# Performance work log

Hardware: AMD Instinct MI355X
Metric: run time of the kernel (lower is better)

Reference implementation:

```python
import jax, jax.numpy as jnp
import numpy as np

SCALING = 32.0 / 16.0  # alpha / r

def setup_inputs() -> dict:
    key = jax.random.key(0)
    k1, k2, k3, k4 = jax.random.split(key, 4)
    B_, S, D_in, D_out, R = 4, 2048, 4096, 4096, 16
    x = jax.random.normal(k1, (B_, S, D_in), dtype=jnp.float32)
    W_base = jax.random.normal(k2, (D_out, D_in), dtype=jnp.float32) * 0.02
    b_base = jax.random.normal(k3, (D_out,), dtype=jnp.float32) * 0.02
    A = jax.random.normal(k4, (R, D_in), dtype=jnp.float32) * 0.02
    B = jnp.zeros((D_out, R), dtype=jnp.float32)  # lora_B init to zeros
    return {"x": x, "W_base": W_base, "b_base": b_base, "A": A, "B": B}

def reference(x, W_base, b_base, A, B):
    # base linear (stands in for dequantized 4-bit matmul): [B,S,Din] @ [Din,Dout]
    out = jnp.einsum('bsd,od->bso', x, W_base) + b_base
    # LoRA path: B(A(x)) * scaling, dropout=0 -> identity
    xa = jnp.einsum('bsd,rd->bsr', x, A)        # [B,S,r]
    delta = jnp.einsum('bsr,or->bso', xa, B)    # [B,S,Dout]
    return out + delta * SCALING
```

## Files before the change

### kernel.cpp

```cpp
#include <hip/hip_runtime.h>


typedef __attribute__((ext_vector_type(4))) float f32x4;
typedef __attribute__((ext_vector_type(8))) short bf16x8;

__device__ __forceinline__ unsigned short f2bf(float f) {
    unsigned u = __builtin_bit_cast(unsigned, f);
    unsigned r = u + 0x7fffu + ((u >> 16) & 1u);
    return (unsigned short)(r >> 16);
}

__device__ __forceinline__ void gload_lds16(const void* g, void* l) {
    __builtin_amdgcn_global_load_lds(
        (const __attribute__((address_space(1))) void*)g,
        (__attribute__((address_space(3))) void*)l, 16, 0, 0);
}

__global__ __launch_bounds__(256) void cast_x_kernel(
    const float* __restrict__ x, unsigned short* __restrict__ xb, int n8)
{
    int stride = gridDim.x * blockDim.x;
    for (int i = blockIdx.x * blockDim.x + threadIdx.x; i < n8; i += stride) {
        size_t base = (size_t)i * 8;
        float4 f0 = *(const float4*)&x[base];
        float4 f1 = *(const float4*)&x[base + 4];
        ushort4 o0, o1;
        o0.x = f2bf(f0.x); o0.y = f2bf(f0.y); o0.z = f2bf(f0.z); o0.w = f2bf(f0.w);
        o1.x = f2bf(f1.x); o1.y = f2bf(f1.y); o1.z = f2bf(f1.z); o1.w = f2bf(f1.w);
        *(ushort4*)&xb[base]     = o0;
        *(ushort4*)&xb[base + 4] = o1;
    }
}

__global__ __launch_bounds__(256) void prep_w_kernel(
    const float* __restrict__ W, const float* __restrict__ A,
    const float* __restrict__ Bl, unsigned short* __restrict__ wb,
    int K, float scale)
{
    __shared__ float Bs[16][16];
    const int t = threadIdx.x;
    const int n0 = blockIdx.y * 16;
    const int k0 = blockIdx.x * 256;
    {
        int nl = t >> 4, r = t & 15;
        Bs[nl][r] = Bl[(size_t)(n0 + nl) * 16 + r];
    }
    __syncthreads();

    const int lane = t & 63;
    const int wv = t >> 6;
    const int k = k0 + lane * 4;

    float4 av[16];
#pragma unroll
    for (int r = 0; r < 16; ++r)
        av[r] = *(const float4*)&A[(size_t)r * K + k];

#pragma unroll
    for (int j = 0; j < 4; ++j) {
        const int nl = wv * 4 + j;
        const int n = n0 + nl;
        float4 w = *(const float4*)&W[(size_t)n * K + k];
        float d0 = 0.f, d1 = 0.f, d2 = 0.f, d3 = 0.f;
#pragma unroll
        for (int r = 0; r < 16; ++r) {
            float b = Bs[nl][r];
            d0 += b * av[r].x; d1 += b * av[r].y;
            d2 += b * av[r].z; d3 += b * av[r].w;
        }
        ushort4 o;
        o.x = f2bf(w.x + scale * d0);
        o.y = f2bf(w.y + scale * d1);
        o.z = f2bf(w.z + scale * d2);
        o.w = f2bf(w.w + scale * d3);
        *(ushort4*)&wb[(size_t)n * K + k] = o;
    }
}


#define SETPRIO(p) __builtin_amdgcn_s_setprio(p)
#define BARRIER()  __builtin_amdgcn_s_barrier()
#define LGKM0()    asm volatile("s_waitcnt lgkmcnt(0)" ::: "memory")

__global__ __launch_bounds__(512, 2) void gemm256_kernel(
    const unsigned short* __restrict__ Xb, const unsigned short* __restrict__ Wb,
    const float* __restrict__ bias, float* __restrict__ out,
    int M, int N, int K)
{
    __shared__ __align__(16) unsigned short lds[2][2][2][8192];

    const int NT = K / 64;
    const int ntn = N / 256;
    int bid = blockIdx.x;
    {
        int per = gridDim.x >> 3;
        bid = (bid & 7) * per + (bid >> 3);
    }
    const int tm = bid / ntn, tn = bid % ntn;

    const int t = threadIdx.x;
    const int lane = t & 63, wave = t >> 6;
    const int wr = wave >> 2;
    const int wc = wave & 3;
    const int wch = wc >> 1;
    const int bro = (wc & 1) * 64;

    const int srow = t >> 3;
    const int scol = ((t & 7) * 8) ^ (((t >> 3) & 7) << 3);
    unsigned gA[2][2], gB[2][2];
#pragma unroll
    for (int h = 0; h < 2; ++h)
#pragma unroll
        for (int i = 0; i < 2; ++i) {
            gA[h][i] = (unsigned)((tm * 256 + h * 128 + i * 64 + srow) * K + scol);
            gB[h][i] = (unsigned)((tn * 256 + h * 128 + i * 64 + srow) * K + scol);
        }

#define ST_A4(buf, ktt)                                                         \
    _Pragma("unroll") for (int h = 0; h < 2; ++h)                               \
    _Pragma("unroll") for (int i = 0; i < 2; ++i)                               \
        gload_lds16(Xb + gA[h][i] + (ktt) * 64,                                 \
                    &lds[buf][0][h][i * 4096 + wave * 512]);
#define ST_B4(buf, ktt)                                                         \
    _Pragma("unroll") for (int h = 0; h < 2; ++h)                               \
    _Pragma("unroll") for (int i = 0; i < 2; ++i)                               \
        gload_lds16(Wb + gB[h][i] + (ktt) * 64,                                 \
                    &lds[buf][1][h][i * 4096 + wave * 512]);

    const int fr = lane & 15;
    const int hi16 = ((lane >> 4) & 3) * 16;
    const int bsw = (fr & 7) << 4;
    const int lo0 = hi16 ^ bsw;
    const int lo1 = (64 + hi16) ^ bsw;

    f32x4 acc[8][4] = {};
    bf16x8 a03[4][2], a47[4][2], b01[2][2], b23[2][2];

    ST_A4(0, 0) ST_B4(0, 0)
    ST_A4(1, 1) ST_B4(1, 1)
    asm volatile("s_waitcnt vmcnt(8)" ::: "memory");
    BARRIER();
    {
        const char* pA = (const char*)&lds[0][0][wr][0];
        const char* pB = (const char*)&lds[0][1][wch][0];
#pragma unroll
        for (int i = 0; i < 4; ++i) {
            a03[i][0] = *(const bf16x8*)(pA + (i * 16 + fr) * 128 + lo0);
            a03[i][1] = *(const bf16x8*)(pA + (i * 16 + fr) * 128 + lo1);
        }
#pragma unroll
        for (int i = 0; i < 2; ++i) {
            b01[i][0] = *(const bf16x8*)(pB + (bro + i * 16 + fr) * 128 + lo0);
            b01[i][1] = *(const bf16x8*)(pB + (bro + i * 16 + fr) * 128 + lo1);
        }
    }

#define MFMA_Q(AV, BV, M0, N0)                                                  \
    _Pragma("unroll") for (int mi = 0; mi < 4; ++mi)                            \
    _Pragma("unroll") for (int ni = 0; ni < 2; ++ni)                            \
    _Pragma("unroll") for (int kk = 0; kk < 2; ++kk)                            \
        acc[(M0) + mi][(N0) + ni] = __builtin_amdgcn_mfma_f32_16x16x32_bf16(    \
            AV[mi][kk], BV[ni][kk], acc[(M0) + mi][(N0) + ni], 0, 0, 0);

    for (int kt = 0; kt < NT; ++kt) {
        const int cur = kt & 1;
        const char* pA  = (const char*)&lds[cur][0][wr][0];
        const char* pB  = (const char*)&lds[cur][1][wch][0];
        const char* pA1 = (const char*)&lds[cur ^ 1][0][wr][0];
        const char* pB1 = (const char*)&lds[cur ^ 1][1][wch][0];
        const bool stB = (kt + 1 < NT);
        const bool stA = (kt + 2 < NT);

        LGKM0();
#pragma unroll
        for (int i = 0; i < 4; ++i) {
            a47[i][0] = *(const bf16x8*)(pA + ((4 + i) * 16 + fr) * 128 + lo0);
            a47[i][1] = *(const bf16x8*)(pA + ((4 + i) * 16 + fr) * 128 + lo1);
        }
        SETPRIO(1);
        MFMA_Q(a03, b01, 0, 0)
        SETPRIO(0);
        BARRIER();

        LGKM0();
#pragma unroll
        for (int i = 0; i < 2; ++i) {
            b23[i][0] = *(const bf16x8*)(pB + (bro + (2 + i) * 16 + fr) * 128 + lo0);
            b23[i][1] = *(const bf16x8*)(pB + (bro + (2 + i) * 16 + fr) * 128 + lo1);
        }
        SETPRIO(1);
        MFMA_Q(a47, b01, 4, 0)
        SETPRIO(0);
        asm volatile("s_waitcnt vmcnt(0)" ::: "memory");
        BARRIER();

        LGKM0();
        if (stB) {
#pragma unroll
            for (int i = 0; i < 2; ++i) {
                b01[i][0] = *(const bf16x8*)(pB1 + (bro + i * 16 + fr) * 128 + lo0);
                b01[i][1] = *(const bf16x8*)(pB1 + (bro + i * 16 + fr) * 128 + lo1);
            }
        }
        if (stA) { ST_A4(cur, kt + 2) }
        SETPRIO(1);
        MFMA_Q(a03, b23, 0, 2)
        SETPRIO(0);
        BARRIER();

        LGKM0();
        if (stB) {
#pragma unroll
            for (int i = 0; i < 4; ++i) {
                a03[i][0] = *(const bf16x8*)(pA1 + (i * 16 + fr) * 128 + lo0);
                a03[i][1] = *(const bf16x8*)(pA1 + (i * 16 + fr) * 128 + lo1);
            }
        }
        if (stA) { ST_B4(cur, kt + 2) }
        SETPRIO(1);
        MFMA_Q(a47, b23, 4, 2)
        SETPRIO(0);
        BARRIER();
    }

    const int row0 = tm * 256 + wr * 128 + (lane >> 4) * 4;
    const int col0 = tn * 256 + wc * 64;
#pragma unroll
    for (int ni = 0; ni < 4; ++ni) {
        const int col = col0 + ni * 16 + fr;
        const float bv = bias[col];
#pragma unroll
        for (int mi = 0; mi < 8; ++mi) {
            const int row = row0 + mi * 16;
#pragma unroll
            for (int r = 0; r < 4; ++r)
                out[(size_t)(row + r) * N + col] = acc[mi][ni][r] + bv;
        }
    }
}

extern "C" void kernel_launch(void* const* d_in, const int* in_sizes, int n_in,
                              void* d_out, int out_size, void* d_ws, size_t ws_size,
                              hipStream_t stream)
{
    const float* x  = (const float*)d_in[0];
    const float* W  = (const float*)d_in[1];
    const float* b  = (const float*)d_in[2];
    const float* A  = (const float*)d_in[3];
    const float* Bl = (const float*)d_in[4];
    float* out = (float*)d_out;

    const int Dout = in_sizes[2];
    const int Din  = in_sizes[1] / Dout;
    const int M    = in_sizes[0] / Din;

    unsigned short* xb = (unsigned short*)d_ws;
    unsigned short* wb = xb + (size_t)M * Din;

    cast_x_kernel<<<2048, 256, 0, stream>>>(x, xb, M * Din / 8);

    dim3 gw(Din / 256, Dout / 16);
    prep_w_kernel<<<gw, 256, 0, stream>>>(W, A, Bl, wb, Din, 2.0f);

    const int grid = (M / 256) * (Dout / 256);
    gemm256_kernel<<<grid, 512, 0, stream>>>(xb, wb, b, out, M, Dout, Din);
}
```

Measured before the change: 301.7 us.

## Cut main-loop barriers to one per K-step and use counted LDS waits

Reworks the GEMM main loop so each K-iteration has a single barrier instead of four. All LDS fragment reads for the current tile are issued up front, and partial lgkmcnt waits (12, 4, 0) let MFMAs start as soon as their operands arrive. Both A and B global→LDS prefetches for tile kt+2 are now issued together after the barrier. The next tile's fragments are read before the final MFMA quarter. The aim is to cut barrier stalls and overlap LDS latency with MFMA. It depends on the in-order LDS counters and may raise register pressure.

```diff
diff --git a/kernel.cpp b/kernel.cpp
--- a/kernel.cpp
+++ b/kernel.cpp
@@ -80,7 +80,7 @@
 
 #define SETPRIO(p) __builtin_amdgcn_s_setprio(p)
 #define BARRIER()  __builtin_amdgcn_s_barrier()
-#define LGKM0()    asm volatile("s_waitcnt lgkmcnt(0)" ::: "memory")
+#define LGKM(n)    asm volatile("s_waitcnt lgkmcnt(" #n ")" ::: "memory")
 
 __global__ __launch_bounds__(512, 2) void gemm256_kernel(
     const unsigned short* __restrict__ Xb, const unsigned short* __restrict__ Wb,
@@ -136,6 +136,34 @@
     f32x4 acc[8][4] = {};
     bf16x8 a03[4][2], a47[4][2], b01[2][2], b23[2][2];
 
+#define RD_A03(P)                                                               \
+    _Pragma("unroll") for (int i = 0; i < 4; ++i) {                             \
+        a03[i][0] = *(const bf16x8*)((P) + (i * 16 + fr) * 128 + lo0);          \
+        a03[i][1] = *(const bf16x8*)((P) + (i * 16 + fr) * 128 + lo1);          \
+    }
+#define RD_A47(P)                                                               \
+    _Pragma("unroll") for (int i = 0; i < 4; ++i) {                             \
+        a47[i][0] = *(const bf16x8*)((P) + ((4 + i) * 16 + fr) * 128 + lo0);    \
+        a47[i][1] = *(const bf16x8*)((P) + ((4 + i) * 16 + fr) * 128 + lo1);    \
+    }
+#define RD_B01(P)                                                               \
+    _Pragma("unroll") for (int i = 0; i < 2; ++i) {                             \
+        b01[i][0] = *(const bf16x8*)((P) + (bro + i * 16 + fr) * 128 + lo0);    \
+        b01[i][1] = *(const bf16x8*)((P) + (bro + i * 16 + fr) * 128 + lo1);    \
+    }
+#define RD_B23(P)                                                               \
+    _Pragma("unroll") for (int i = 0; i < 2; ++i) {                             \
+        b23[i][0] = *(const bf16x8*)((P) + (bro + (2+i) * 16 + fr) * 128 + lo0);\
+        b23[i][1] = *(const bf16x8*)((P) + (bro + (2+i) * 16 + fr) * 128 + lo1);\
+    }
+
+#define MFMA_Q(AV, BV, M0, N0)                                                  \
+    _Pragma("unroll") for (int mi = 0; mi < 4; ++mi)                            \
+    _Pragma("unroll") for (int ni = 0; ni < 2; ++ni)                            \
+    _Pragma("unroll") for (int kk = 0; kk < 2; ++kk)                            \
+        acc[(M0) + mi][(N0) + ni] = __builtin_amdgcn_mfma_f32_16x16x32_bf16(    \
+            AV[mi][kk], BV[ni][kk], acc[(M0) + mi][(N0) + ni], 0, 0, 0);
+
     ST_A4(0, 0) ST_B4(0, 0)
     ST_A4(1, 1) ST_B4(1, 1)
     asm volatile("s_waitcnt vmcnt(8)" ::: "memory");
@@ -143,24 +171,9 @@
     {
         const char* pA = (const char*)&lds[0][0][wr][0];
         const char* pB = (const char*)&lds[0][1][wch][0];
-#pragma unroll
-        for (int i = 0; i < 4; ++i) {
-            a03[i][0] = *(const bf16x8*)(pA + (i * 16 + fr) * 128 + lo0);
-            a03[i][1] = *(const bf16x8*)(pA + (i * 16 + fr) * 128 + lo1);
-        }
-#pragma unroll
-        for (int i = 0; i < 2; ++i) {
-            b01[i][0] = *(const bf16x8*)(pB + (bro + i * 16 + fr) * 128 + lo0);
-            b01[i][1] = *(const bf16x8*)(pB + (bro + i * 16 + fr) * 128 + lo1);
-        }
-    }
-
-#define MFMA_Q(AV, BV, M0, N0)                                                  \
-    _Pragma("unroll") for (int mi = 0; mi < 4; ++mi)                            \
-    _Pragma("unroll") for (int ni = 0; ni < 2; ++ni)                            \
-    _Pragma("unroll") for (int kk = 0; kk < 2; ++kk)                            \
-        acc[(M0) + mi][(N0) + ni] = __builtin_amdgcn_mfma_f32_16x16x32_bf16(    \
-            AV[mi][kk], BV[ni][kk], acc[(M0) + mi][(N0) + ni], 0, 0, 0);
+        RD_A03(pA)
+        RD_B01(pB)
+    }
 
     for (int kt = 0; kt < NT; ++kt) {
         const int cur = kt & 1;
@@ -168,59 +181,35 @@
         const char* pB  = (const char*)&lds[cur][1][wch][0];
         const char* pA1 = (const char*)&lds[cur ^ 1][0][wr][0];
         const char* pB1 = (const char*)&lds[cur ^ 1][1][wch][0];
-        const bool stB = (kt + 1 < NT);
-        const bool stA = (kt + 2 < NT);
-
-        LGKM0();
-#pragma unroll
-        for (int i = 0; i < 4; ++i) {
-            a47[i][0] = *(const bf16x8*)(pA + ((4 + i) * 16 + fr) * 128 + lo0);
-            a47[i][1] = *(const bf16x8*)(pA + ((4 + i) * 16 + fr) * 128 + lo1);
-        }
+
+        RD_A47(pA)
+        RD_B23(pB)
+
+        LGKM(12);
         SETPRIO(1);
         MFMA_Q(a03, b01, 0, 0)
         SETPRIO(0);
-        BARRIER();
-
-        LGKM0();
-#pragma unroll
-        for (int i = 0; i < 2; ++i) {
-            b23[i][0] = *(const bf16x8*)(pB + (bro + (2 + i) * 16 + fr) * 128 + lo0);
-            b23[i][1] = *(const bf16x8*)(pB + (bro + (2 + i) * 16 + fr) * 128 + lo1);
-        }
+
+        LGKM(4);
         SETPRIO(1);
         MFMA_Q(a47, b01, 4, 0)
         SETPRIO(0);
+
+        LGKM(0);
         asm volatile("s_waitcnt vmcnt(0)" ::: "memory");
         BARRIER();
 
-        LGKM0();
-        if (stB) {
-#pragma unroll
-            for (int i = 0; i < 2; ++i) {
-                b01[i][0] = *(const bf16x8*)(pB1 + (bro + i * 16 + fr) * 128 + lo0);
-                b01[i][1] = *(const bf16x8*)(pB1 + (bro + i * 16 + fr) * 128 + lo1);
-            }
-        }
-        if (stA) { ST_A4(cur, kt + 2) }
+        if (kt + 2 < NT) { ST_A4(cur, kt + 2) ST_B4(cur, kt + 2) }
+
         SETPRIO(1);
         MFMA_Q(a03, b23, 0, 2)
         SETPRIO(0);
-        BARRIER();
-
-        LGKM0();
-        if (stB) {
-#pragma unroll
-            for (int i = 0; i < 4; ++i) {
-                a03[i][0] = *(const bf16x8*)(pA1 + (i * 16 + fr) * 128 + lo0);
-                a03[i][1] = *(const bf16x8*)(pA1 + (i * 16 + fr) * 128 + lo1);
-            }
-        }
-        if (stA) { ST_B4(cur, kt + 2) }
+
+        if (kt + 1 < NT) { RD_B01(pB1) RD_A03(pA1) }
+
         SETPRIO(1);
         MFMA_Q(a47, b23, 4, 2)
         SETPRIO(0);
-        BARRIER();
     }
 
     const int row0 = tm * 256 + wr * 128 + (lane >> 4) * 4;
```

After: 301.9 us. Within noise of the previous version (+0.1%).
